# Optimization experiments

Measured on AMD Instinct MI355X. Metric: run time of the kernel, lower is better.

The kernel has to match this reference:

```python
import jax, jax.numpy as jnp
import numpy as np

N_HEADS = 8
HEAD_DIM = 64  # d_model // n_heads = 512 // 8


def setup_inputs() -> dict:
    key = jax.random.key(0)
    kq, kk, kv, km = jax.random.split(key, 4)
    B, C, H, L, D = 8, 4, N_HEADS, 512, HEAD_DIM
    q = jax.random.normal(kq, (B * C, H, L, D), dtype=jnp.float32)
    k = jax.random.normal(kk, (B * C, H, D, L), dtype=jnp.float32)  # pre-transposed, matmul(q, k) directly
    v = jax.random.normal(kv, (B * C, H, L, D), dtype=jnp.float32)
    attn_mask = jax.random.randint(km, (B, L, L), 0, 2).astype(bool)  # True = masked out
    return {"q": q, "k": k, "v": v, "attn_mask": attn_mask}


def reference(q, k, v, attn_mask):
    # q: [B*C, H, L, D]; k: [B*C, H, D, L]; v: [B*C, H, L, D]; attn_mask: [B, L, L] bool
    scale = jnp.asarray(HEAD_DIM ** (-0.5), dtype=q.dtype)
    scores = jnp.einsum('ghld,ghdm->ghlm', q, k) * scale  # [B*C, H, L, L]
    if attn_mask is not None:
        B = attn_mask.shape[0]
        C = q.shape[0] // B
        H, L = scores.shape[1], scores.shape[2]
        scores = scores.reshape(B, C, H, L, L)
        mask = attn_mask[:, None, None, :, :]  # broadcast over channels and heads
        scores = jnp.where(mask, -jnp.inf, scores)
        scores = scores.reshape(B * C, H, L, L)
    attn_weights = jax.nn.softmax(scores, axis=-1)  # dropout p=0.0 -> identity (eval)
    output = jnp.einsum('ghlm,ghmd->ghld', attn_weights, v)  # [B*C, H, L, D]
    return output
```

## Files before the change

### kernel.cpp

```cpp
#include <hip/hip_runtime.h>


typedef __attribute__((ext_vector_type(8)))  short bf16x8;
typedef __attribute__((ext_vector_type(16))) float f32x16;

union Frag4 { uint4 x; unsigned u[4]; bf16x8 v; };

__device__ __forceinline__ unsigned pk_bf16(float a, float b){
    unsigned ua = __builtin_bit_cast(unsigned, a) + 0x8000u;
    unsigned ub = __builtin_bit_cast(unsigned, b) + 0x8000u;
    return __builtin_amdgcn_perm(ub, ua, 0x07060302u);
}

__device__ __forceinline__ float fast_exp2(float x){
#if __has_builtin(__builtin_amdgcn_exp2f)
    return __builtin_amdgcn_exp2f(x);
#else
    return exp2f(x);
#endif
}

#define L2E 1.44269504088896f

__global__ __launch_bounds__(256)
void pack_mask(const int* __restrict__ mg, unsigned long long* __restrict__ bits)
{
    const int t    = blockIdx.x*256 + threadIdx.x;
    const int lane = t & 63;
    const int w0   = t >> 6;
    const int strd = (int)((gridDim.x*256) >> 6);
    const int nW   = 8*512*8;
    for (int i = w0; i < nW; i += strd){
        int v = mg[(size_t)i*64 + lane];
        unsigned long long m = __ballot(v != 0);
        if (lane == 0) bits[i] = m;
    }
}

template<int BITS>
__global__ __launch_bounds__(256, 4)
void attn_fused(const float* __restrict__ qg, const float* __restrict__ kg,
                const float* __restrict__ vg, const int* __restrict__ mg,
                const unsigned* __restrict__ bits, float* __restrict__ og)
{
    __shared__ uint4 sKt4[64*8];
    __shared__ uint4 sVt4[64*8];

    const int t    = threadIdx.x;
    const int lane = t & 63;
    const int wv   = t >> 6;
    const int col  = lane & 31;
    const int h    = lane >> 5;

    const int bi   = blockIdx.x;
    const int s    = bi >> 3;
    const int head = (bi & 7)*32 + (s >> 2);
    const int qt   = s & 3;
    const int b    = bi & 7;

    const float* qh = qg + (size_t)head*32768;
    const float* kh = kg + (size_t)head*32768;
    const float* vh = vg + (size_t)head*32768;
    float*       oh = og + (size_t)head*32768;

    const int qrl = wv*32 + col;
    const int* mrow0 = BITS ? nullptr
        : mg + (size_t)b*262144 + (size_t)(qt*128 + qrl)*512;
    const unsigned* brow = BITS
        ? bits + ((size_t)b*512 + qt*128 + qrl)*16
        : nullptr;

    Frag4 qf[4];
    {
        const float* qr = qh + (size_t)(qt*128 + qrl)*64 + h*8;
        #pragma unroll
        for (int kt=0; kt<4; ++kt){
            float4 x0 = *(const float4*)(qr + kt*16);
            float4 x1 = *(const float4*)(qr + kt*16 + 4);
            qf[kt].u[0] = pk_bf16(x0.x*0.125f, x0.y*0.125f);
            qf[kt].u[1] = pk_bf16(x0.z*0.125f, x0.w*0.125f);
            qf[kt].u[2] = pk_bf16(x1.x*0.125f, x1.y*0.125f);
            qf[kt].u[3] = pk_bf16(x1.z*0.125f, x1.w*0.125f);
        }
    }

    f32x16 o0, o1;
    #pragma unroll
    for (int i=0;i<16;++i){ o0[i]=0.f; o1[i]=0.f; }
    float lsum = 0.f;

    for (int kb=0; kb<8; ++kb){
        __syncthreads();

        uint2 mbv;
        if constexpr (BITS) mbv = *(const uint2*)(brow + kb*2);

        #pragma unroll
        for (int gi=0; gi<2; ++gi){
            const int g = wv + gi*4;
            const float* kp = kh + (size_t)(g*8)*512 + kb*64 + lane;
            float kv[8];
            #pragma unroll
            for (int dd=0; dd<8; ++dd) kv[dd] = kp[(size_t)dd*512];
            Frag4 w;
            w.u[0]=pk_bf16(kv[0],kv[1]); w.u[1]=pk_bf16(kv[2],kv[3]);
            w.u[2]=pk_bf16(kv[4],kv[5]); w.u[3]=pk_bf16(kv[6],kv[7]);
            sKt4[lane*8 + (g ^ (lane&7))] = w.x;
        }
        #pragma unroll
        for (int gi=0; gi<2; ++gi){
            const int g = wv + gi*4;
            const float* vp = vh + (size_t)(kb*64 + g*8)*64 + lane;
            float vv[8];
            #pragma unroll
            for (int mm=0; mm<8; ++mm) vv[mm] = vp[(size_t)mm*64];
            Frag4 w;
            w.u[0]=pk_bf16(vv[0],vv[1]); w.u[1]=pk_bf16(vv[2],vv[3]);
            w.u[2]=pk_bf16(vv[4],vv[5]); w.u[3]=pk_bf16(vv[6],vv[7]);
            sVt4[lane*8 + (g ^ (lane&7))] = w.x;
        }
        __syncthreads();

        #pragma unroll
        for (int mt=0; mt<2; ++mt){
            f32x16 sc;
            #pragma unroll
            for (int i=0;i<16;++i) sc[i]=0.f;
            #pragma unroll
            for (int kt=0; kt<4; ++kt){
                const int r = mt*32 + col;
                Frag4 a; a.x = sKt4[r*8 + ((kt*2+h) ^ (r&7))];
                sc = __builtin_amdgcn_mfma_f32_32x32x16_bf16(a.v, qf[kt].v, sc, 0, 0, 0);
            }
            float p[16];
            if constexpr (BITS){
                const unsigned mword = mt ? mbv.y : mbv.x;
                #pragma unroll
                for (int rg=0; rg<4; ++rg){
                    const unsigned mw = mword >> (rg*8 + h*4);
                    float e0 = (mw & 1u) ? 0.f : fast_exp2(sc[4*rg+0]*L2E);
                    float e1 = (mw & 2u) ? 0.f : fast_exp2(sc[4*rg+1]*L2E);
                    float e2 = (mw & 4u) ? 0.f : fast_exp2(sc[4*rg+2]*L2E);
                    float e3 = (mw & 8u) ? 0.f : fast_exp2(sc[4*rg+3]*L2E);
                    p[4*rg+0]=e0; p[4*rg+1]=e1; p[4*rg+2]=e2; p[4*rg+3]=e3;
                    lsum += (e0+e1)+(e2+e3);
                }
            } else {
                const int* mrow = mrow0 + kb*64;
                #pragma unroll
                for (int rg=0; rg<4; ++rg){
                    int4 mm = *(const int4*)(mrow + mt*32 + rg*8 + h*4);
                    float e0 = mm.x ? 0.f : fast_exp2(sc[4*rg+0]*L2E);
                    float e1 = mm.y ? 0.f : fast_exp2(sc[4*rg+1]*L2E);
                    float e2 = mm.z ? 0.f : fast_exp2(sc[4*rg+2]*L2E);
                    float e3 = mm.w ? 0.f : fast_exp2(sc[4*rg+3]*L2E);
                    p[4*rg+0]=e0; p[4*rg+1]=e1; p[4*rg+2]=e2; p[4*rg+3]=e3;
                    lsum += (e0+e1)+(e2+e3);
                }
            }
            unsigned pp[8];
            #pragma unroll
            for (int r2=0; r2<8; ++r2) pp[r2] = pk_bf16(p[2*r2], p[2*r2+1]);

            #pragma unroll
            for (int c=0; c<2; ++c){
                unsigned keep0 = h ? pp[4*c+2] : pp[4*c+0];
                unsigned keep1 = h ? pp[4*c+3] : pp[4*c+1];
                unsigned give0 = h ? pp[4*c+0] : pp[4*c+2];
                unsigned give1 = h ? pp[4*c+1] : pp[4*c+3];
                unsigned got0 = (unsigned)__shfl_xor((int)give0, 32, 64);
                unsigned got1 = (unsigned)__shfl_xor((int)give1, 32, 64);
                Frag4 pa;
                pa.u[0] = h ? got0  : keep0;
                pa.u[1] = h ? got1  : keep1;
                pa.u[2] = h ? keep0 : got0;
                pa.u[3] = h ? keep1 : got1;
                const int gm = mt*4 + c*2 + h;
                Frag4 b0; b0.x = sVt4[col*8      + (gm ^ (col&7))];
                o0 = __builtin_amdgcn_mfma_f32_32x32x16_bf16(pa.v, b0.v, o0, 0, 0, 0);
                Frag4 b1; b1.x = sVt4[(32+col)*8 + (gm ^ ((32+col)&7))];
                o1 = __builtin_amdgcn_mfma_f32_32x32x16_bf16(pa.v, b1.v, o1, 0, 0, 0);
            }
        }
    }

    lsum += __shfl_xor(lsum, 32, 64);
    const float inv = 1.0f / lsum;
    float* ob = oh + (size_t)(qt*128 + wv*32)*64;
    #pragma unroll
    for (int r=0; r<16; ++r){
        const int qq = (r&3) + 8*(r>>2) + 4*h;
        const float iv = __shfl(inv, qq, 64);
        ob[(size_t)qq*64 + col]      = o0[r]*iv;
        ob[(size_t)qq*64 + 32 + col] = o1[r]*iv;
    }
}

extern "C" void kernel_launch(void* const* d_in, const int* in_sizes, int n_in,
                              void* d_out, int out_size, void* d_ws, size_t ws_size,
                              hipStream_t stream) {
    (void)in_sizes; (void)n_in; (void)out_size;
    const float* q = (const float*)d_in[0];
    const float* k = (const float*)d_in[1];
    const float* v = (const float*)d_in[2];
    const int*   m = (const int*)d_in[3];
    const size_t BITS_BYTES = (size_t)8*512*64;
    if (d_ws && ws_size >= BITS_BYTES){
        pack_mask<<<dim3(1024), dim3(256), 0, stream>>>(m, (unsigned long long*)d_ws);
        attn_fused<1><<<dim3(1024), dim3(256), 0, stream>>>(
            q, k, v, m, (const unsigned*)d_ws, (float*)d_out);
    } else {
        attn_fused<0><<<dim3(1024), dim3(256), 0, stream>>>(
            q, k, v, m, nullptr, (float*)d_out);
    }
}
```

Measured before the change: 169.2 us.

## Double-buffer K/V tiles in LDS with register prefetch of the next block

K and V staging now uses two LDS buffers. The next key block's global loads are issued into registers before the current block's MFMA work and written to the alternate buffer afterward, so only one barrier per iteration remains and global latency overlaps compute. It also raises wave priority around the MFMA sequences and packs the probabilities to bf16 inline. In exchange it doubles LDS use and adds 32 live registers per thread, which may reduce occupancy under the four-blocks-per-CU launch bound. The final iteration also loads an unneeded wrapped-around block.

New measurement: 198.0 us. 17.0% more time.

```diff
diff --git a/kernel.cpp b/kernel.cpp
--- a/kernel.cpp
+++ b/kernel.cpp
@@ -37,14 +37,47 @@
     }
 }
 
+#define STAGE_LOAD(kbx, kf, vf)                                               \
+    {                                                                         \
+        _Pragma("unroll")                                                     \
+        for (int gi=0; gi<2; ++gi){                                           \
+            const float* kp_ = kh + (size_t)((wv + gi*4)*8)*512 + (kbx)*64 + lane; \
+            _Pragma("unroll")                                                 \
+            for (int dd=0; dd<8; ++dd) kf[gi*8+dd] = kp_[(size_t)dd*512];     \
+            const float* vp_ = vh + (size_t)((kbx)*64 + (wv + gi*4)*8)*64 + lane;  \
+            _Pragma("unroll")                                                 \
+            for (int mm=0; mm<8; ++mm) vf[gi*8+mm] = vp_[(size_t)mm*64];      \
+        }                                                                     \
+    }
+
+#define STAGE_WRITE(buf, kf, vf)                                              \
+    {                                                                         \
+        _Pragma("unroll")                                                     \
+        for (int gi=0; gi<2; ++gi){                                           \
+            const int g_ = wv + gi*4;                                         \
+            Frag4 wk_;                                                        \
+            wk_.u[0]=pk_bf16(kf[gi*8+0],kf[gi*8+1]);                          \
+            wk_.u[1]=pk_bf16(kf[gi*8+2],kf[gi*8+3]);                          \
+            wk_.u[2]=pk_bf16(kf[gi*8+4],kf[gi*8+5]);                          \
+            wk_.u[3]=pk_bf16(kf[gi*8+6],kf[gi*8+7]);                          \
+            sKt4[buf][lane*8 + (g_ ^ (lane&7))] = wk_.x;                      \
+            Frag4 wv_;                                                        \
+            wv_.u[0]=pk_bf16(vf[gi*8+0],vf[gi*8+1]);                          \
+            wv_.u[1]=pk_bf16(vf[gi*8+2],vf[gi*8+3]);                          \
+            wv_.u[2]=pk_bf16(vf[gi*8+4],vf[gi*8+5]);                          \
+            wv_.u[3]=pk_bf16(vf[gi*8+6],vf[gi*8+7]);                          \
+            sVt4[buf][lane*8 + (g_ ^ (lane&7))] = wv_.x;                      \
+        }                                                                     \
+    }
+
 template<int BITS>
 __global__ __launch_bounds__(256, 4)
 void attn_fused(const float* __restrict__ qg, const float* __restrict__ kg,
                 const float* __restrict__ vg, const int* __restrict__ mg,
                 const unsigned* __restrict__ bits, float* __restrict__ og)
 {
-    __shared__ uint4 sKt4[64*8];
-    __shared__ uint4 sVt4[64*8];
+    __shared__ uint4 sKt4[2][64*8];
+    __shared__ uint4 sVt4[2][64*8];
 
     const int t    = threadIdx.x;
     const int lane = t & 63;
@@ -89,50 +122,38 @@
     for (int i=0;i<16;++i){ o0[i]=0.f; o1[i]=0.f; }
     float lsum = 0.f;
 
+    {
+        float k0[16], v0[16];
+        STAGE_LOAD(0, k0, v0);
+        STAGE_WRITE(0, k0, v0);
+    }
+    __syncthreads();
+
     for (int kb=0; kb<8; ++kb){
-        __syncthreads();
+        const int cur = kb & 1;
+        const int nx  = (kb+1) & 7;
 
         uint2 mbv;
         if constexpr (BITS) mbv = *(const uint2*)(brow + kb*2);
-
-        #pragma unroll
-        for (int gi=0; gi<2; ++gi){
-            const int g = wv + gi*4;
-            const float* kp = kh + (size_t)(g*8)*512 + kb*64 + lane;
-            float kv[8];
-            #pragma unroll
-            for (int dd=0; dd<8; ++dd) kv[dd] = kp[(size_t)dd*512];
-            Frag4 w;
-            w.u[0]=pk_bf16(kv[0],kv[1]); w.u[1]=pk_bf16(kv[2],kv[3]);
-            w.u[2]=pk_bf16(kv[4],kv[5]); w.u[3]=pk_bf16(kv[6],kv[7]);
-            sKt4[lane*8 + (g ^ (lane&7))] = w.x;
-        }
-        #pragma unroll
-        for (int gi=0; gi<2; ++gi){
-            const int g = wv + gi*4;
-            const float* vp = vh + (size_t)(kb*64 + g*8)*64 + lane;
-            float vv[8];
-            #pragma unroll
-            for (int mm=0; mm<8; ++mm) vv[mm] = vp[(size_t)mm*64];
-            Frag4 w;
-            w.u[0]=pk_bf16(vv[0],vv[1]); w.u[1]=pk_bf16(vv[2],vv[3]);
-            w.u[2]=pk_bf16(vv[4],vv[5]); w.u[3]=pk_bf16(vv[6],vv[7]);
-            sVt4[lane*8 + (g ^ (lane&7))] = w.x;
-        }
-        __syncthreads();
+        float kn[16], vn[16];
+        STAGE_LOAD(nx, kn, vn);
+        __builtin_amdgcn_sched_barrier(0);
 
         #pragma unroll
         for (int mt=0; mt<2; ++mt){
             f32x16 sc;
             #pragma unroll
             for (int i=0;i<16;++i) sc[i]=0.f;
+            __builtin_amdgcn_s_setprio(1);
             #pragma unroll
             for (int kt=0; kt<4; ++kt){
                 const int r = mt*32 + col;
-                Frag4 a; a.x = sKt4[r*8 + ((kt*2+h) ^ (r&7))];
+                Frag4 a; a.x = sKt4[cur][r*8 + ((kt*2+h) ^ (r&7))];
                 sc = __builtin_amdgcn_mfma_f32_32x32x16_bf16(a.v, qf[kt].v, sc, 0, 0, 0);
             }
-            float p[16];
+            __builtin_amdgcn_s_setprio(0);
+
+            unsigned pp[8];
             if constexpr (BITS){
                 const unsigned mword = mt ? mbv.y : mbv.x;
                 #pragma unroll
@@ -142,8 +163,9 @@
                     float e1 = (mw & 2u) ? 0.f : fast_exp2(sc[4*rg+1]*L2E);
                     float e2 = (mw & 4u) ? 0.f : fast_exp2(sc[4*rg+2]*L2E);
                     float e3 = (mw & 8u) ? 0.f : fast_exp2(sc[4*rg+3]*L2E);
-                    p[4*rg+0]=e0; p[4*rg+1]=e1; p[4*rg+2]=e2; p[4*rg+3]=e3;
                     lsum += (e0+e1)+(e2+e3);
+                    pp[2*rg]   = pk_bf16(e0, e1);
+                    pp[2*rg+1] = pk_bf16(e2, e3);
                 }
             } else {
                 const int* mrow = mrow0 + kb*64;
@@ -154,13 +176,11 @@
                     float e1 = mm.y ? 0.f : fast_exp2(sc[4*rg+1]*L2E);
                     float e2 = mm.z ? 0.f : fast_exp2(sc[4*rg+2]*L2E);
                     float e3 = mm.w ? 0.f : fast_exp2(sc[4*rg+3]*L2E);
-                    p[4*rg+0]=e0; p[4*rg+1]=e1; p[4*rg+2]=e2; p[4*rg+3]=e3;
                     lsum += (e0+e1)+(e2+e3);
+                    pp[2*rg]   = pk_bf16(e0, e1);
+                    pp[2*rg+1] = pk_bf16(e2, e3);
                 }
             }
-            unsigned pp[8];
-            #pragma unroll
-            for (int r2=0; r2<8; ++r2) pp[r2] = pk_bf16(p[2*r2], p[2*r2+1]);
 
             #pragma unroll
             for (int c=0; c<2; ++c){
@@ -176,12 +196,18 @@
                 pa.u[2] = h ? keep0 : got0;
                 pa.u[3] = h ? keep1 : got1;
                 const int gm = mt*4 + c*2 + h;
-                Frag4 b0; b0.x = sVt4[col*8      + (gm ^ (col&7))];
+                Frag4 b0; b0.x = sVt4[cur][col*8      + (gm ^ (col&7))];
+                Frag4 b1; b1.x = sVt4[cur][(32+col)*8 + (gm ^ ((32+col)&7))];
+                __builtin_amdgcn_s_setprio(1);
                 o0 = __builtin_amdgcn_mfma_f32_32x32x16_bf16(pa.v, b0.v, o0, 0, 0, 0);
-                Frag4 b1; b1.x = sVt4[(32+col)*8 + (gm ^ ((32+col)&7))];
                 o1 = __builtin_amdgcn_mfma_f32_32x32x16_bf16(pa.v, b1.v, o1, 0, 0, 0);
+                __builtin_amdgcn_s_setprio(0);
             }
         }
+
+        __builtin_amdgcn_sched_barrier(0);
+        STAGE_WRITE(cur^1, kn, vn);
+        __syncthreads();
     }
 
     lsum += __shfl_xor(lsum, 32, 64);
```

## Halve query tile per block to 64 rows with 2048 blocks of 128 threads

Applied to the files above, without the earlier changes.

Each block now handles 64 query rows using 2 waves instead of 128 rows with 4 waves, and the grid doubles to 2048 blocks. Each wave therefore loads 4 K/V groups into shared memory per iteration instead of 2. Because each block covers half as many query rows, every K/V tile is loaded and converted to bf16 twice as often across the grid. The softmax probabilities are packed to bf16 inline rather than through a temporary array. A build_mword helper is added but never called.

Result: slower. 194.4 us (+14.9%).

```diff
diff --git a/kernel.cpp b/kernel.cpp
--- a/kernel.cpp
+++ b/kernel.cpp
@@ -37,8 +37,22 @@
     }
 }
 
+__device__ __forceinline__ unsigned build_mword(const int* p, int h){
+    unsigned w = 0;
+    #pragma unroll
+    for (int rg=0; rg<4; ++rg){
+        int4 mm = *(const int4*)(p + rg*8 + h*4);
+        const unsigned base = rg*8 + h*4;
+        w |= (mm.x?1u:0u) << base;
+        w |= (mm.y?1u:0u) << (base+1);
+        w |= (mm.z?1u:0u) << (base+2);
+        w |= (mm.w?1u:0u) << (base+3);
+    }
+    return w;
+}
+
 template<int BITS>
-__global__ __launch_bounds__(256, 4)
+__global__ __launch_bounds__(128, 4)
 void attn_fused(const float* __restrict__ qg, const float* __restrict__ kg,
                 const float* __restrict__ vg, const int* __restrict__ mg,
                 const unsigned* __restrict__ bits, float* __restrict__ og)
@@ -54,8 +68,8 @@
 
     const int bi   = blockIdx.x;
     const int s    = bi >> 3;
-    const int head = (bi & 7)*32 + (s >> 2);
-    const int qt   = s & 3;
+    const int head = (bi & 7)*32 + (s >> 3);
+    const int qt   = s & 7;
     const int b    = bi & 7;
 
     const float* qh = qg + (size_t)head*32768;
@@ -63,16 +77,17 @@
     const float* vh = vg + (size_t)head*32768;
     float*       oh = og + (size_t)head*32768;
 
-    const int qrl = wv*32 + col;
+    const int qrl  = wv*32 + col;
+    const int qrow = qt*64 + qrl;
     const int* mrow0 = BITS ? nullptr
-        : mg + (size_t)b*262144 + (size_t)(qt*128 + qrl)*512;
+        : mg + (size_t)b*262144 + (size_t)qrow*512;
     const unsigned* brow = BITS
-        ? bits + ((size_t)b*512 + qt*128 + qrl)*16
+        ? bits + ((size_t)b*512 + qrow)*16
         : nullptr;
 
     Frag4 qf[4];
     {
-        const float* qr = qh + (size_t)(qt*128 + qrl)*64 + h*8;
+        const float* qr = qh + (size_t)qrow*64 + h*8;
         #pragma unroll
         for (int kt=0; kt<4; ++kt){
             float4 x0 = *(const float4*)(qr + kt*16);
@@ -96,8 +111,8 @@
         if constexpr (BITS) mbv = *(const uint2*)(brow + kb*2);
 
         #pragma unroll
-        for (int gi=0; gi<2; ++gi){
-            const int g = wv + gi*4;
+        for (int gi=0; gi<4; ++gi){
+            const int g = wv*4 + gi;
             const float* kp = kh + (size_t)(g*8)*512 + kb*64 + lane;
             float kv[8];
             #pragma unroll
@@ -108,8 +123,8 @@
             sKt4[lane*8 + (g ^ (lane&7))] = w.x;
         }
         #pragma unroll
-        for (int gi=0; gi<2; ++gi){
-            const int g = wv + gi*4;
+        for (int gi=0; gi<4; ++gi){
+            const int g = wv*4 + gi;
             const float* vp = vh + (size_t)(kb*64 + g*8)*64 + lane;
             float vv[8];
             #pragma unroll
@@ -121,6 +136,7 @@
         }
         __syncthreads();
 
+        const int* mrow = BITS ? nullptr : (mrow0 + kb*64);
         #pragma unroll
         for (int mt=0; mt<2; ++mt){
             f32x16 sc;
@@ -132,7 +148,7 @@
                 Frag4 a; a.x = sKt4[r*8 + ((kt*2+h) ^ (r&7))];
                 sc = __builtin_amdgcn_mfma_f32_32x32x16_bf16(a.v, qf[kt].v, sc, 0, 0, 0);
             }
-            float p[16];
+            unsigned pp[8];
             if constexpr (BITS){
                 const unsigned mword = mt ? mbv.y : mbv.x;
                 #pragma unroll
@@ -142,11 +158,11 @@
                     float e1 = (mw & 2u) ? 0.f : fast_exp2(sc[4*rg+1]*L2E);
                     float e2 = (mw & 4u) ? 0.f : fast_exp2(sc[4*rg+2]*L2E);
                     float e3 = (mw & 8u) ? 0.f : fast_exp2(sc[4*rg+3]*L2E);
-                    p[4*rg+0]=e0; p[4*rg+1]=e1; p[4*rg+2]=e2; p[4*rg+3]=e3;
                     lsum += (e0+e1)+(e2+e3);
+                    pp[2*rg]   = pk_bf16(e0, e1);
+                    pp[2*rg+1] = pk_bf16(e2, e3);
                 }
             } else {
-                const int* mrow = mrow0 + kb*64;
                 #pragma unroll
                 for (int rg=0; rg<4; ++rg){
                     int4 mm = *(const int4*)(mrow + mt*32 + rg*8 + h*4);
@@ -154,13 +170,11 @@
                     float e1 = mm.y ? 0.f : fast_exp2(sc[4*rg+1]*L2E);
                     float e2 = mm.z ? 0.f : fast_exp2(sc[4*rg+2]*L2E);
                     float e3 = mm.w ? 0.f : fast_exp2(sc[4*rg+3]*L2E);
-                    p[4*rg+0]=e0; p[4*rg+1]=e1; p[4*rg+2]=e2; p[4*rg+3]=e3;
                     lsum += (e0+e1)+(e2+e3);
+                    pp[2*rg]   = pk_bf16(e0, e1);
+                    pp[2*rg+1] = pk_bf16(e2, e3);
                 }
             }
-            unsigned pp[8];
-            #pragma unroll
-            for (int r2=0; r2<8; ++r2) pp[r2] = pk_bf16(p[2*r2], p[2*r2+1]);
 
             #pragma unroll
             for (int c=0; c<2; ++c){
@@ -186,7 +200,7 @@
 
     lsum += __shfl_xor(lsum, 32, 64);
     const float inv = 1.0f / lsum;
-    float* ob = oh + (size_t)(qt*128 + wv*32)*64;
+    float* ob = oh + (size_t)(qt*64 + wv*32)*64;
     #pragma unroll
     for (int r=0; r<16; ++r){
         const int qq = (r&3) + 8*(r>>2) + 4*h;
@@ -207,10 +221,10 @@
     const size_t BITS_BYTES = (size_t)8*512*64;
     if (d_ws && ws_size >= BITS_BYTES){
         pack_mask<<<dim3(1024), dim3(256), 0, stream>>>(m, (unsigned long long*)d_ws);
-        attn_fused<1><<<dim3(1024), dim3(256), 0, stream>>>(
+        attn_fused<1><<<dim3(2048), dim3(128), 0, stream>>>(
             q, k, v, m, (const unsigned*)d_ws, (float*)d_out);
     } else {
-        attn_fused<0><<<dim3(1024), dim3(256), 0, stream>>>(
+        attn_fused<0><<<dim3(2048), dim3(128), 0, stream>>>(
             q, k, v, m, nullptr, (float*)d_out);
     }
 }
```
